# Performance work log

Hardware: AMD Instinct MI355X
Metric: run time of the kernel (lower is better)

Reference implementation:

```python
import jax, jax.numpy as jnp
import numpy as np
import math

N_HEADS = 16
D_EMB = 1024
D_HEAD = D_EMB // N_HEADS


def setup_inputs() -> dict:
    key = jax.random.key(0)
    ks = jax.random.split(key, 5)
    scale_in = 1.0 / math.sqrt(D_EMB)
    x = jax.random.normal(ks[0], (2, 2048, D_EMB), dtype=jnp.float32)
    w_in = jax.random.uniform(ks[1], (3 * D_EMB, D_EMB), dtype=jnp.float32, minval=-scale_in, maxval=scale_in)
    b_in = jax.random.uniform(ks[2], (3 * D_EMB,), dtype=jnp.float32, minval=-scale_in, maxval=scale_in)
    w_out = jax.random.uniform(ks[3], (D_EMB, D_EMB), dtype=jnp.float32, minval=-scale_in, maxval=scale_in)
    b_out = jax.random.uniform(ks[4], (D_EMB,), dtype=jnp.float32, minval=-scale_in, maxval=scale_in)
    return {"x": x, "w_in": w_in, "b_in": b_in, "w_out": w_out, "b_out": b_out, "apply_mask": 1}


def reference(x, w_in, b_in, w_out, b_out, apply_mask):
    B, S, D = x.shape
    # fused QKV projection: torch Linear uses y = x @ W^T + b
    qkv = jnp.einsum('bsd,ed->bse', x, w_in) + b_in  # [B,S,3D]
    q, k, v = jnp.split(qkv, 3, axis=-1)
    # [B,H,S,Dh]
    q = q.reshape(B, S, N_HEADS, D_HEAD).transpose(0, 2, 1, 3)
    k = k.reshape(B, S, N_HEADS, D_HEAD).transpose(0, 2, 1, 3)
    v = v.reshape(B, S, N_HEADS, D_HEAD).transpose(0, 2, 1, 3)
    w = jnp.einsum('bhqd,bhkd->bhqk', q, k)  # [B,H,S,S]
    if apply_mask:
        causal = jnp.triu(jnp.ones((S, S), dtype=bool), k=1)
        w = jnp.where(causal, -jnp.inf, w)
    w = w / jnp.sqrt(jnp.float32(D_HEAD)).astype(w.dtype)
    w = jax.nn.softmax(w, axis=-1)
    score = jnp.einsum('bhqk,bhkd->bhqd', w, v)  # [B,H,S,Dh]
    score = score.transpose(0, 2, 1, 3).reshape(B, S, D)
    return jnp.einsum('bsd,ed->bse', score, w_out) + b_out
```

## Files before the change

### kernel.cpp

```cpp
#include <hip/hip_runtime.h>
#include <stdint.h>

#define DEMB 1024
#define NHEAD 16
#define DHEAD 64
#define SEQ 2048
#define MROWS 4096

typedef __bf16 bf16x8 __attribute__((ext_vector_type(8)));
typedef float f32x4 __attribute__((ext_vector_type(4)));
typedef unsigned short u16;

#define LOG2E 1.44269504088896340736f

__device__ __forceinline__ u16 f2b(float f) {
  return __builtin_bit_cast(u16, (__bf16)f);
}
__device__ __forceinline__ uint32_t pk2(float a, float b) {
  return (uint32_t)f2b(a) | ((uint32_t)f2b(b) << 16);
}

__device__ __forceinline__ f32x4 mfma16(bf16x8 a, bf16x8 b, f32x4 c) {
  return __builtin_amdgcn_mfma_f32_16x16x32_bf16(a, b, c, 0, 0, 0);
}

__device__ __forceinline__ void gload_lds16(const void* g, void* l) {
  __builtin_amdgcn_global_load_lds(
      (__attribute__((address_space(1))) unsigned int*)(g),
      (__attribute__((address_space(3))) unsigned int*)(l), 16, 0, 0);
}

__device__ __forceinline__ void tile_barrier() {
  __builtin_amdgcn_sched_barrier(0);
  asm volatile("s_waitcnt vmcnt(0) lgkmcnt(0)" ::: "memory");
  __builtin_amdgcn_s_barrier();
  __builtin_amdgcn_sched_barrier(0);
}

__global__ void cvt3_f32_bf16(const float* __restrict__ a, int na,
                              const float* __restrict__ b, int nb,
                              const float* __restrict__ c, int nc,
                              u16* __restrict__ da, u16* __restrict__ db,
                              u16* __restrict__ dc) {
  const int total = (na + nb + nc) >> 2;
  const int stride = gridDim.x * blockDim.x;
  for (int t = blockIdx.x * blockDim.x + threadIdx.x; t < total; t += stride) {
    int i = t << 2;
    const float* s;
    u16* d;
    if (i < na) {
      s = a + i; d = da + i;
    } else if (i < na + nb) {
      s = b + (i - na); d = db + (i - na);
    } else {
      s = c + (i - na - nb); d = dc + (i - na - nb);
    }
    float4 f = *(const float4*)s;
    ushort4 o;
    o.x = f2b(f.x); o.y = f2b(f.y); o.z = f2b(f.z); o.w = f2b(f.w);
    *(ushort4*)d = o;
  }
}

template <int EPI>
__global__ __launch_bounds__(256, 2) void gemm_nt(
    const u16* __restrict__ A, const u16* __restrict__ Bw,
    const float* __restrict__ bias, int K, int N,
    u16* __restrict__ q_out, u16* __restrict__ k_out, u16* __restrict__ v_out,
    float* __restrict__ f_out) {
  __shared__ __align__(16) u16 As[128 * 64];
  __shared__ __align__(16) u16 Bs[128 * 64];
  const int tid = threadIdx.x;
  const int w = tid >> 6;
  const int lane = tid & 63;
  const int wm = w >> 1, wn = w & 1;
  const int m0 = blockIdx.y * 128, n0 = blockIdx.x * 128;
  const int l16 = lane & 15, lg = lane >> 4;
  const int st_row = lane >> 3, st_slot = lane & 7;

  f32x4 acc[4][4] = {};

  for (int k0 = 0; k0 < K; k0 += 64) {
#pragma unroll
    for (int i = 0; i < 4; ++i) {
      const int chunk = (w << 2) | i;
      const int row = (chunk << 3) | st_row;
      const int scol = (st_slot ^ (row & 7)) << 3;
      gload_lds16(A + (size_t)(m0 + row) * K + k0 + scol, (char*)As + (chunk << 10));
      gload_lds16(Bw + (size_t)(n0 + row) * K + k0 + scol, (char*)Bs + (chunk << 10));
    }
    __syncthreads();
#pragma unroll
    for (int ks = 0; ks < 2; ++ks) {
      bf16x8 af[4], bfr[4];
#pragma unroll
      for (int mi = 0; mi < 4; ++mi) {
        const int row = wm * 64 + mi * 16 + l16;
        const int cb = ((ks << 6) | (lg << 4)) ^ ((row & 7) << 4);
        af[mi] = *(const bf16x8*)((const char*)As + row * 128 + cb);
      }
#pragma unroll
      for (int ni = 0; ni < 4; ++ni) {
        const int row = wn * 64 + ni * 16 + l16;
        const int cb = ((ks << 6) | (lg << 4)) ^ ((row & 7) << 4);
        bfr[ni] = *(const bf16x8*)((const char*)Bs + row * 128 + cb);
      }
#pragma unroll
      for (int mi = 0; mi < 4; ++mi)
#pragma unroll
        for (int ni = 0; ni < 4; ++ni)
          acc[mi][ni] = mfma16(af[mi], bfr[ni], acc[mi][ni]);
    }
    __syncthreads();
  }

#pragma unroll
  for (int ni = 0; ni < 4; ++ni) {
    const int n = n0 + wn * 64 + ni * 16 + l16;
    const float bv = bias[n];
    if (EPI == 0) {
      const int part = n >> 10;
      const int hh = (n >> 6) & 15;
      const int dh = n & 63;
      const float scl = (part == 0) ? (0.125f * LOG2E) : 1.0f;
      u16* dst = (part == 0) ? q_out : (part == 1) ? k_out : v_out;
#pragma unroll
      for (int mi = 0; mi < 4; ++mi) {
#pragma unroll
        for (int i = 0; i < 4; ++i) {
          const int m = m0 + wm * 64 + mi * 16 + (lg << 2) + i;
          const int bq = m >> 11, s = m & 2047;
          dst[((size_t)((bq << 4) | hh) * SEQ + s) * DHEAD + dh] = f2b((acc[mi][ni][i] + bv) * scl);
        }
      }
    } else {
#pragma unroll
      for (int mi = 0; mi < 4; ++mi)
#pragma unroll
        for (int i = 0; i < 4; ++i) {
          const int m = m0 + wm * 64 + mi * 16 + (lg << 2) + i;
          f_out[(size_t)m * N + n] = acc[mi][ni][i] + bv;
        }
    }
  }
}

__device__ __forceinline__ int swz4(int r) { return (r ^ (r >> 3)) & 15; }

__device__ __forceinline__ void stage_k(const u16* __restrict__ Kb, size_t base,
                                        int jt, u16* Ks, int w, int lane) {
#pragma unroll
  for (int i = 0; i < 4; ++i) {
    const int g = (w << 2) | i;
    const int row = (g << 2) | (lane >> 4);
    const int shat = (lane & 15) ^ swz4(row);
    const int kv = (row << 1) | (shat >> 3);
    const int del = (shat & 7) << 3;
    gload_lds16(Kb + base + (size_t)(jt * 128 + kv) * DHEAD + del,
                (char*)Ks + (g << 10));
  }
}

__device__ __forceinline__ void write_vt(u16* Vt, const uint4* v, int tid) {
  const int c0 = (tid & 7) << 3;
  const int vrb = tid >> 3;
#pragma unroll
  for (int k = 0; k < 4; ++k) {
    const int vr = vrb + (k << 5);
    const u16* pv = (const u16*)&v[k];
#pragma unroll
    for (int e = 0; e < 8; ++e) {
      const int rt = c0 + e;
      *(u16*)((char*)Vt + rt * 256 + ((vr << 1) ^ (swz4(rt) << 4))) = pv[e];
    }
  }
}

__global__ __launch_bounds__(256, 2) void attn_fwd(
    const u16* __restrict__ Qb, const u16* __restrict__ Kb,
    const u16* __restrict__ Vb, u16* __restrict__ Ob,
    const int* __restrict__ amask) {
  __shared__ __align__(16) u16 Ks[2][64 * 128];
  __shared__ __align__(16) u16 Vt[2][64 * 128];
  __shared__ __align__(16) uint32_t Ps[4][1024];
  const int tid = threadIdx.x;
  const int w = tid >> 6, lane = tid & 63;
  const int l16 = lane & 15, lg = lane >> 4;

  const int id = blockIdx.x;
  const int xcd = id & 7;
  const int r = id >> 3;
  const int bh = (xcd << 2) | (r & 3);
  const int p = r >> 2;
  const int qiA = 31 - p, qiB = p;

  const size_t base = (size_t)bh * (SEQ * DHEAD);
  const bool causal = (amask[0] != 0);
  const int ntA = causal ? ((qiA >> 1) + 1) : (SEQ / 128);
  const int ntB = causal ? ((qiB >> 1) + 1) : (SEQ / 128);
  const int nt = ntA + ntB;
  const int b = bh >> 4, h = bh & 15;

  int qseg0 = qiA * 64;

  bf16x8 qf[2];
  {
    const u16* qp = Qb + base + (size_t)(qseg0 + (w << 4) + l16) * DHEAD + (lg << 3);
    qf[0] = *(const bf16x8*)qp;
    qf[1] = *(const bf16x8*)(qp + 32);
  }

  float mrow = -1e30f, lrow = 0.f;
  f32x4 oacc[4] = {};

  const int vcol = (tid & 7) << 3;
  const int vrow = tid >> 3;
  const int key = (l16 & 7) << 2;
  char* prow = (char*)(&Ps[w][0]) + l16 * 256;

  stage_k(Kb, base, 0, Ks[0], w, lane);
  {
    uint4 v[4];
#pragma unroll
    for (int k = 0; k < 4; ++k)
      v[k] = *(const uint4*)(Vb + base + (size_t)(vrow + (k << 5)) * DHEAD + vcol);
    write_vt(Vt[0], v, tid);
  }
  tile_barrier();

  int cur = 0;
  for (int t = 0; t < nt; ++t) {
    const int j = (t >= ntA) ? (t - ntA) : t;
    const u16* Kcur = Ks[cur];
    const u16* Vcur = Vt[cur];
    const bool pre = (t + 1 < nt);
    uint4 vn[4] = {};
    if (pre) {
      const int jn = (t + 1 >= ntA) ? (t + 1 - ntA) : (t + 1);
      stage_k(Kb, base, jn, Ks[cur ^ 1], w, lane);
      const u16* vsrc = Vb + base + (size_t)jn * 128 * DHEAD;
#pragma unroll
      for (int k = 0; k < 4; ++k)
        vn[k] = *(const uint4*)(vsrc + (size_t)(vrow + (k << 5)) * DHEAD + vcol);
    }

    f32x4 sv[8];
    __builtin_amdgcn_s_setprio(1);
#pragma unroll
    for (int nf = 0; nf < 8; ++nf) {
      const int row2 = (nf << 3) | (l16 >> 1);
      const int sz = swz4(row2);
      const int s0 = ((l16 & 1) << 3) | lg;
      bf16x8 kf0 = *(const bf16x8*)((const char*)Kcur + row2 * 256 + ((s0 ^ sz) << 4));
      bf16x8 kf1 = *(const bf16x8*)((const char*)Kcur + row2 * 256 + (((s0 | 4) ^ sz) << 4));
      f32x4 s = {};
      s = mfma16(kf0, qf[0], s);
      s = mfma16(kf1, qf[1], s);
      sv[nf] = s;
    }
    __builtin_amdgcn_s_setprio(0);

    const bool segEnd = (t == ntA - 1) || (t == nt - 1);
    if (causal && segEnd) {
      const int q = qseg0 + (w << 4) + l16;
#pragma unroll
      for (int nf = 0; nf < 8; ++nf)
#pragma unroll
        for (int i = 0; i < 4; ++i) {
          const int kv = j * 128 + (nf << 4) + (lg << 2) + i;
          if (kv > q) sv[nf][i] = -1e30f;
        }
    }

    float tmax;
    {
      f32x4 m01, m23, m45, m67, ma, mb, mt;
#pragma unroll
      for (int i = 0; i < 4; ++i) {
        m01[i] = fmaxf(sv[0][i], sv[1][i]);
        m23[i] = fmaxf(sv[2][i], sv[3][i]);
        m45[i] = fmaxf(sv[4][i], sv[5][i]);
        m67[i] = fmaxf(sv[6][i], sv[7][i]);
        ma[i] = fmaxf(m01[i], m23[i]);
        mb[i] = fmaxf(m45[i], m67[i]);
        mt[i] = fmaxf(ma[i], mb[i]);
      }
      tmax = fmaxf(fmaxf(mt[0], mt[1]), fmaxf(mt[2], mt[3]));
      tmax = fmaxf(tmax, __shfl_xor(tmax, 16));
      tmax = fmaxf(tmax, __shfl_xor(tmax, 32));
    }

    if (__any(tmax > mrow + 8.0f)) {
      const float mnew = fmaxf(mrow, tmax);
      const float corr = __builtin_amdgcn_exp2f(mrow - mnew);
      mrow = mnew;
      lrow *= corr;
#pragma unroll
      for (int df = 0; df < 4; ++df)
#pragma unroll
        for (int i = 0; i < 4; ++i) oacc[df][i] *= corr;
    }

    float ps0 = 0.f, ps1 = 0.f;
#pragma unroll
    for (int nf = 0; nf < 8; ++nf) {
      const float p0 = __builtin_amdgcn_exp2f(sv[nf][0] - mrow);
      const float p1 = __builtin_amdgcn_exp2f(sv[nf][1] - mrow);
      const float p2 = __builtin_amdgcn_exp2f(sv[nf][2] - mrow);
      const float p3 = __builtin_amdgcn_exp2f(sv[nf][3] - mrow);
      ps0 += p0 + p1;
      ps1 += p2 + p3;
      uint2 pkv;
      pkv.x = pk2(p0, p1);
      pkv.y = pk2(p2, p3);
      const int word = ((nf << 3) | (lg << 1)) ^ key;
      *(uint2*)(prow + word * 4) = pkv;
    }
    float psum = ps0 + ps1;
    psum += __shfl_xor(psum, 16);
    psum += __shfl_xor(psum, 32);
    lrow += psum;

    bf16x8 pa[4];
#pragma unroll
    for (int s = 0; s < 4; ++s)
      pa[s] = *(const bf16x8*)(prow + ((((s << 4) | (lg << 2)) ^ key) << 2));

    __builtin_amdgcn_s_setprio(1);
#pragma unroll
    for (int df = 0; df < 4; ++df) {
      const int row = (df << 4) + l16;
      const int sz = swz4(row) << 4;
#pragma unroll
      for (int s = 0; s < 4; ++s) {
        bf16x8 vf = *(const bf16x8*)((const char*)Vcur + row * 256 + (((s << 6) | (lg << 4)) ^ sz));
        oacc[df] = mfma16(vf, pa[s], oacc[df]);
      }
    }
    __builtin_amdgcn_s_setprio(0);

    if (segEnd) {
      const float inv = 1.0f / lrow;
      const int s = qseg0 + (w << 4) + l16;
      u16* orow = Ob + (size_t)(b * SEQ + s) * DEMB + h * DHEAD;
#pragma unroll
      for (int df = 0; df < 4; ++df) {
        ushort4 o;
        o.x = f2b(oacc[df][0] * inv);
        o.y = f2b(oacc[df][1] * inv);
        o.z = f2b(oacc[df][2] * inv);
        o.w = f2b(oacc[df][3] * inv);
        *(ushort4*)(orow + (df << 4) + (lg << 2)) = o;
      }
      if (t != nt - 1) {
        qseg0 = qiB * 64;
        mrow = -1e30f;
        lrow = 0.f;
#pragma unroll
        for (int df = 0; df < 4; ++df)
#pragma unroll
          for (int i = 0; i < 4; ++i) oacc[df][i] = 0.f;
        const u16* qp = Qb + base + (size_t)(qseg0 + (w << 4) + l16) * DHEAD + (lg << 3);
        qf[0] = *(const bf16x8*)qp;
        qf[1] = *(const bf16x8*)(qp + 32);
      }
    }

    if (pre) {
      write_vt(Vt[cur ^ 1], vn, tid);
      tile_barrier();
    }
    cur ^= 1;
  }
}

extern "C" void kernel_launch(void* const* d_in, const int* in_sizes, int n_in,
                              void* d_out, int out_size, void* d_ws, size_t ws_size,
                              hipStream_t stream) {
  const float* x = (const float*)d_in[0];
  const float* w_in = (const float*)d_in[1];
  const float* b_in = (const float*)d_in[2];
  const float* w_out = (const float*)d_in[3];
  const float* b_out = (const float*)d_in[4];
  const int* amask = (const int*)d_in[5];
  float* out = (float*)d_out;

  u16* xb = (u16*)d_ws;
  u16* wib = xb + (size_t)MROWS * DEMB;
  u16* wob = wib + (size_t)3 * DEMB * DEMB;
  u16* Qb = wob + (size_t)DEMB * DEMB;
  u16* Kb = Qb + (size_t)MROWS * DEMB;
  u16* Vb = Kb + (size_t)MROWS * DEMB;
  u16* Ab = xb;

  cvt3_f32_bf16<<<2048, 256, 0, stream>>>(x, MROWS * DEMB, w_in, 3 * DEMB * DEMB,
                                          w_out, DEMB * DEMB, xb, wib, wob);

  gemm_nt<0><<<dim3(24, 32), 256, 0, stream>>>(xb, wib, b_in, DEMB, 3 * DEMB,
                                               Qb, Kb, Vb, nullptr);
  attn_fwd<<<512, 256, 0, stream>>>(Qb, Kb, Vb, Ab, amask);
  gemm_nt<1><<<dim3(8, 32), 256, 0, stream>>>(Ab, wob, b_out, DEMB, DEMB,
                                              nullptr, nullptr, nullptr, out);
}
```

Measured before the change: 111.8 us.

## Emit V pre-transposed from QKV GEMM and stage it via direct LDS loads

The QKV projection epilogue now writes V in a transposed [b,h,dh,s] layout with 4-element vector stores. The attention kernel loads V tiles straight into LDS with the same async global-to-LDS swizzled path used for K. This replaces the register-staged V load and the per-element scattered LDS transpose writes. The aim is to cut VALU/LDS work and register pressure in the attention loop and to let V loads overlap compute like K. The trade-off is that the GEMM epilogue's V stores become strided across the sequence dimension.

```diff
diff --git a/kernel.cpp b/kernel.cpp
--- a/kernel.cpp
+++ b/kernel.cpp
@@ -122,15 +122,29 @@
       const int part = n >> 10;
       const int hh = (n >> 6) & 15;
       const int dh = n & 63;
-      const float scl = (part == 0) ? (0.125f * LOG2E) : 1.0f;
-      u16* dst = (part == 0) ? q_out : (part == 1) ? k_out : v_out;
-#pragma unroll
-      for (int mi = 0; mi < 4; ++mi) {
-#pragma unroll
-        for (int i = 0; i < 4; ++i) {
-          const int m = m0 + wm * 64 + mi * 16 + (lg << 2) + i;
-          const int bq = m >> 11, s = m & 2047;
-          dst[((size_t)((bq << 4) | hh) * SEQ + s) * DHEAD + dh] = f2b((acc[mi][ni][i] + bv) * scl);
+      if (part == 2) {
+#pragma unroll
+        for (int mi = 0; mi < 4; ++mi) {
+          const int mbase = m0 + wm * 64 + mi * 16 + (lg << 2);
+          const int bq = mbase >> 11, s0 = mbase & 2047;
+          ushort4 o;
+          o.x = f2b(acc[mi][ni][0] + bv);
+          o.y = f2b(acc[mi][ni][1] + bv);
+          o.z = f2b(acc[mi][ni][2] + bv);
+          o.w = f2b(acc[mi][ni][3] + bv);
+          *(ushort4*)(v_out + ((size_t)(((bq << 4) | hh) * 64 + dh)) * SEQ + s0) = o;
+        }
+      } else {
+        const float scl = (part == 0) ? (0.125f * LOG2E) : 1.0f;
+        u16* dst = (part == 0) ? q_out : k_out;
+#pragma unroll
+        for (int mi = 0; mi < 4; ++mi) {
+#pragma unroll
+          for (int i = 0; i < 4; ++i) {
+            const int m = m0 + wm * 64 + mi * 16 + (lg << 2) + i;
+            const int bq = m >> 11, s = m & 2047;
+            dst[((size_t)((bq << 4) | hh) * SEQ + s) * DHEAD + dh] = f2b((acc[mi][ni][i] + bv) * scl);
+          }
         }
       }
     } else {
@@ -161,24 +175,21 @@
   }
 }
 
-__device__ __forceinline__ void write_vt(u16* Vt, const uint4* v, int tid) {
-  const int c0 = (tid & 7) << 3;
-  const int vrb = tid >> 3;
-#pragma unroll
-  for (int k = 0; k < 4; ++k) {
-    const int vr = vrb + (k << 5);
-    const u16* pv = (const u16*)&v[k];
-#pragma unroll
-    for (int e = 0; e < 8; ++e) {
-      const int rt = c0 + e;
-      *(u16*)((char*)Vt + rt * 256 + ((vr << 1) ^ (swz4(rt) << 4))) = pv[e];
-    }
+__device__ __forceinline__ void stage_v(const u16* __restrict__ VTg, size_t base,
+                                        int jt, u16* Vs, int w, int lane) {
+#pragma unroll
+  for (int i = 0; i < 4; ++i) {
+    const int g = (w << 2) | i;
+    const int row = (g << 2) | (lane >> 4);
+    const int shat = (lane & 15) ^ swz4(row);
+    gload_lds16(VTg + base + (size_t)row * SEQ + jt * 128 + (shat << 3),
+                (char*)Vs + (g << 10));
   }
 }
 
 __global__ __launch_bounds__(256, 2) void attn_fwd(
     const u16* __restrict__ Qb, const u16* __restrict__ Kb,
-    const u16* __restrict__ Vb, u16* __restrict__ Ob,
+    const u16* __restrict__ VTg, u16* __restrict__ Ob,
     const int* __restrict__ amask) {
   __shared__ __align__(16) u16 Ks[2][64 * 128];
   __shared__ __align__(16) u16 Vt[2][64 * 128];
@@ -213,19 +224,11 @@
   float mrow = -1e30f, lrow = 0.f;
   f32x4 oacc[4] = {};
 
-  const int vcol = (tid & 7) << 3;
-  const int vrow = tid >> 3;
   const int key = (l16 & 7) << 2;
   char* prow = (char*)(&Ps[w][0]) + l16 * 256;
 
   stage_k(Kb, base, 0, Ks[0], w, lane);
-  {
-    uint4 v[4];
-#pragma unroll
-    for (int k = 0; k < 4; ++k)
-      v[k] = *(const uint4*)(Vb + base + (size_t)(vrow + (k << 5)) * DHEAD + vcol);
-    write_vt(Vt[0], v, tid);
-  }
+  stage_v(VTg, base, 0, Vt[0], w, lane);
   tile_barrier();
 
   int cur = 0;
@@ -234,14 +237,10 @@
     const u16* Kcur = Ks[cur];
     const u16* Vcur = Vt[cur];
     const bool pre = (t + 1 < nt);
-    uint4 vn[4] = {};
     if (pre) {
       const int jn = (t + 1 >= ntA) ? (t + 1 - ntA) : (t + 1);
       stage_k(Kb, base, jn, Ks[cur ^ 1], w, lane);
-      const u16* vsrc = Vb + base + (size_t)jn * 128 * DHEAD;
-#pragma unroll
-      for (int k = 0; k < 4; ++k)
-        vn[k] = *(const uint4*)(vsrc + (size_t)(vrow + (k << 5)) * DHEAD + vcol);
+      stage_v(VTg, base, jn, Vt[cur ^ 1], w, lane);
     }
 
     f32x4 sv[8];
@@ -366,10 +365,7 @@
       }
     }
 
-    if (pre) {
-      write_vt(Vt[cur ^ 1], vn, tid);
-      tile_barrier();
-    }
+    if (pre) tile_barrier();
     cur ^= 1;
   }
 }
@@ -390,15 +386,15 @@
   u16* wob = wib + (size_t)3 * DEMB * DEMB;
   u16* Qb = wob + (size_t)DEMB * DEMB;
   u16* Kb = Qb + (size_t)MROWS * DEMB;
-  u16* Vb = Kb + (size_t)MROWS * DEMB;
+  u16* Vtg = Kb + (size_t)MROWS * DEMB;
   u16* Ab = xb;
 
   cvt3_f32_bf16<<<2048, 256, 0, stream>>>(x, MROWS * DEMB, w_in, 3 * DEMB * DEMB,
                                           w_out, DEMB * DEMB, xb, wib, wob);
 
   gemm_nt<0><<<dim3(24, 32), 256, 0, stream>>>(xb, wib, b_in, DEMB, 3 * DEMB,
-                                               Qb, Kb, Vb, nullptr);
-  attn_fwd<<<512, 256, 0, stream>>>(Qb, Kb, Vb, Ab, amask);
+                                               Qb, Kb, Vtg, nullptr);
+  attn_fwd<<<512, 256, 0, stream>>>(Qb, Kb, Vtg, Ab, amask);
   gemm_nt<1><<<dim3(8, 32), 256, 0, stream>>>(Ab, wob, b_out, DEMB, DEMB,
                                               nullptr, nullptr, nullptr, out);
 }
```

Result: faster. 102.2 us (-8.6%).
